# Kernel tuning notes

Measured on AMD Instinct MI355X. Metric: run time of the kernel, lower is better.

The kernel has to match this reference:

```python
import jax, jax.numpy as jnp
import numpy as np

HEADS = 8
HEAD_DIM = 64
SCALE = HEAD_DIM ** -0.5


def setup_inputs() -> dict:
    key = jax.random.key(0)
    k1, k2, k3 = jax.random.split(key, 3)
    b, p, n, dim = 8, 16, 256, 384
    inner = HEADS * HEAD_DIM  # 512
    x = jax.random.normal(k1, (b, p, n, dim), dtype=jnp.float32)
    w_qkv = jax.random.normal(k2, (dim, 3 * inner), dtype=jnp.float32) * (dim ** -0.5)
    w_out = jax.random.normal(k3, (inner, dim), dtype=jnp.float32) * (inner ** -0.5)
    b_out = jnp.zeros((dim,), dtype=jnp.float32)
    return {"x": x, "w_qkv": w_qkv, "w_out": w_out, "b_out": b_out}


def reference(x, w_qkv, w_out, b_out):
    b, p, n, dim = x.shape
    inner = HEADS * HEAD_DIM
    qkv = jnp.einsum('bpnd,de->bpne', x, w_qkv)  # [b,p,n,3*inner]
    q, k, v = jnp.split(qkv, 3, axis=-1)
    # [b,p,n,inner] -> [b,p,h,n,hd]
    def to_heads(t):
        return t.reshape(b, p, n, HEADS, HEAD_DIM).transpose(0, 1, 3, 2, 4)
    q, k, v = to_heads(q), to_heads(k), to_heads(v)
    dots = jnp.einsum('bphqd,bphkd->bphqk', q, k) * SCALE
    attn = jax.nn.softmax(dots, axis=-1)
    out = jnp.einsum('bphqk,bphkd->bphqd', attn, v)
    out = out.transpose(0, 1, 3, 2, 4).reshape(b, p, n, inner)
    return jnp.einsum('bpni,id->bpnd', out, w_out) + b_out
```

## Files before the change

### kernel.cpp

```cpp
#include <hip/hip_runtime.h>
#include <stdint.h>

#define DEVFN __device__ __forceinline__

typedef __attribute__((ext_vector_type(8))) __bf16 bf16x8;
typedef __attribute__((ext_vector_type(8))) short short8;
typedef __attribute__((ext_vector_type(4))) float f32x4;

DEVFN unsigned short f2bf(float f) {
  union { float f; unsigned u; } v; v.f = f;
  return (unsigned short)((v.u + 0x7FFFu + ((v.u >> 16) & 1u)) >> 16);
}

DEVFN void gload_lds16(const void* g, void* l) {
  __builtin_amdgcn_global_load_lds(
      (const __attribute__((address_space(1))) void*)(uintptr_t)g,
      (__attribute__((address_space(3))) void*)(uint32_t)(uintptr_t)l,
      16, 0, 0);
}


__global__ void k_cast_x(const float* __restrict__ x, short* __restrict__ xb, int n8) {
  int i = blockIdx.x * blockDim.x + threadIdx.x;
  if (i >= n8) return;
  const f32x4* xf = (const f32x4*)x;
  f32x4 a = xf[2 * i], b = xf[2 * i + 1];
  short8 s;
  s[0] = (short)f2bf(a[0]); s[1] = (short)f2bf(a[1]);
  s[2] = (short)f2bf(a[2]); s[3] = (short)f2bf(a[3]);
  s[4] = (short)f2bf(b[0]); s[5] = (short)f2bf(b[1]);
  s[6] = (short)f2bf(b[2]); s[7] = (short)f2bf(b[3]);
  ((short8*)xb)[i] = s;
}

__global__ void k_transpose_bf(const float* __restrict__ w, short* __restrict__ wt, int R, int C) {
  int i = blockIdx.x * blockDim.x + threadIdx.x;
  if (i >= R * C) return;
  int c = i / R, r = i - c * R;
  wt[i] = (short)f2bf(w[(size_t)r * C + c]);
}


template <int BF16_OUT>
__global__ __launch_bounds__(256, 3)
void k_gemm(const short* __restrict__ A, const short* __restrict__ Bt,
            unsigned short* __restrict__ Cb, float* __restrict__ Cf,
            const float* __restrict__ bias, int M, int N, int K) {
  __shared__ short As[3][128 * 32];
  __shared__ short Bs[3][128 * 32];
  const int tid = threadIdx.x;
  const int l = tid & 63, w = tid >> 6;
  const int ntile = N >> 7;
  const int nwg = gridDim.x, cpx = nwg >> 3;
  const int bid = (blockIdx.x & 7) * cpx + (blockIdx.x >> 3);
  const int mt = bid / ntile, nt = bid % ntile;
  const int m0 = mt << 7, n0 = nt << 7;
  const int wm = (w >> 1) << 6, wn = (w & 1) << 6;

  f32x4 acc[4][4];
#pragma unroll
  for (int i = 0; i < 4; i++)
#pragma unroll
    for (int j = 0; j < 4; j++) acc[i][j] = (f32x4){0.f, 0.f, 0.f, 0.f};

  const int nsteps = K >> 5;

  auto stage = [&](int buf, int t) {
#pragma unroll
    for (int c = 0; c < 2; ++c) {
      int ch = tid + c * 256;
      int row = ch >> 2, slot = ch & 3;
      gload_lds16(A + (size_t)(m0 + row) * K + t * 32 + slot * 8, &As[buf][ch * 8]);
      gload_lds16(Bt + (size_t)(n0 + row) * K + t * 32 + slot * 8, &Bs[buf][ch * 8]);
    }
  };
  auto compute = [&](int buf) {
    bf16x8 af[4], bfr[4];
#pragma unroll
    for (int i = 0; i < 4; i++) {
      af[i]  = *(const bf16x8*)&As[buf][(wm + i * 16 + (l & 15)) * 32 + (l >> 4) * 8];
      bfr[i] = *(const bf16x8*)&Bs[buf][(wn + i * 16 + (l & 15)) * 32 + (l >> 4) * 8];
    }
#pragma unroll
    for (int i = 0; i < 4; i++)
#pragma unroll
      for (int j = 0; j < 4; j++)
        acc[i][j] = __builtin_amdgcn_mfma_f32_16x16x32_bf16(af[i], bfr[j], acc[i][j], 0, 0, 0);
  };

  stage(0, 0);
  stage(1, 1);
#pragma unroll 1
  for (int t = 0; t < nsteps; ++t) {
    if (t + 1 < nsteps) {
      asm volatile("s_waitcnt vmcnt(4)" ::: "memory");
    } else {
      asm volatile("s_waitcnt vmcnt(0)" ::: "memory");
    }
    __builtin_amdgcn_sched_barrier(0);
    __builtin_amdgcn_s_barrier();
    __builtin_amdgcn_sched_barrier(0);
    if (t + 2 < nsteps) stage((t + 2) % 3, t + 2);
    compute(t % 3);
  }

#pragma unroll
  for (int i = 0; i < 4; i++) {
    int mrow = m0 + wm + i * 16 + ((l >> 4) << 2);
#pragma unroll
    for (int j = 0; j < 4; j++) {
      int ncol = n0 + wn + j * 16 + (l & 15);
#pragma unroll
      for (int r = 0; r < 4; r++) {
        if (BF16_OUT) {
          Cb[(size_t)(mrow + r) * N + ncol] = f2bf(acc[i][j][r]);
        } else {
          Cf[(size_t)(mrow + r) * N + ncol] = acc[i][j][r] + bias[ncol];
        }
      }
    }
  }
}


__global__ void k_attn(const short* __restrict__ qkv, unsigned short* __restrict__ O) {
  __shared__ short Kl[256 * 64];
  __shared__ short Vt[64 * 256];
  __shared__ short Pc[8][16 * 40];

  const int tid = threadIdx.x, l = tid & 63, w = tid >> 6;
  const int bh = blockIdx.x;
  const int bp = bh >> 3, h = bh & 7;
  const size_t tokbase = (size_t)bp * 256 * 1536;
  const int qoff = h * 64, koff = 512 + h * 64, voff = 1024 + h * 64;

#pragma unroll
  for (int c = 0; c < 4; ++c) {
    int ch = tid + c * 512;
    int row = ch >> 3, s = ch & 7;
    int sg = s ^ (row & 7);
    gload_lds16(qkv + tokbase + (size_t)row * 1536 + koff + sg * 8, &Kl[ch * 8]);
  }
#pragma unroll
  for (int c = 0; c < 4; ++c) {
    int ch = tid + c * 512;
    int row = ch >> 3, d0 = (ch & 7) * 8;
    short8 v = *(const short8*)(qkv + tokbase + (size_t)row * 1536 + voff + d0);
#pragma unroll
    for (int j = 0; j < 8; ++j) {
      int d = d0 + j;
      Vt[d * 256 + (((((row >> 3) ^ (d & 15))) << 3) | (row & 7))] = v[j];
    }
  }
  __syncthreads();

  const float CEXP = 0.125f * 1.44269504f;

#pragma unroll 1
  for (int it = 0; it < 2; ++it) {
    const int q0 = w * 32 + it * 16;
    bf16x8 qa[2];
#pragma unroll
    for (int dc = 0; dc < 2; ++dc)
      qa[dc] = *(const bf16x8*)(qkv + tokbase + (size_t)(q0 + (l & 15)) * 1536 + qoff +
                                dc * 32 + (l >> 4) * 8);
    f32x4 s[16];
#pragma unroll
    for (int kt = 0; kt < 16; kt++) s[kt] = (f32x4){0.f, 0.f, 0.f, 0.f};
#pragma unroll
    for (int dc = 0; dc < 2; ++dc) {
#pragma unroll
      for (int kt = 0; kt < 16; ++kt) {
        int kcol = kt * 16 + (l & 15);
        int sl = (dc * 4 + (l >> 4)) ^ (kcol & 7);
        bf16x8 kb = *(const bf16x8*)&Kl[kcol * 64 + sl * 8];
        s[kt] = __builtin_amdgcn_mfma_f32_16x16x32_bf16(qa[dc], kb, s[kt], 0, 0, 0);
      }
    }
    float rs[4];
#pragma unroll
    for (int r = 0; r < 4; ++r) {
      float m = s[0][r];
#pragma unroll
      for (int kt = 1; kt < 16; kt++) m = fmaxf(m, s[kt][r]);
      for (int off = 1; off < 16; off <<= 1) m = fmaxf(m, __shfl_xor(m, off, 64));
      float sum = 0.f;
#pragma unroll
      for (int kt = 0; kt < 16; kt++) {
        float p = exp2f((s[kt][r] - m) * CEXP);
        s[kt][r] = p;
        sum += p;
      }
      for (int off = 1; off < 16; off <<= 1) sum += __shfl_xor(sum, off, 64);
      rs[r] = 1.0f / sum;
    }
    f32x4 o[4];
#pragma unroll
    for (int dt = 0; dt < 4; dt++) o[dt] = (f32x4){0.f, 0.f, 0.f, 0.f};
    short* pc = &Pc[w][0];
#pragma unroll
    for (int kc = 0; kc < 8; ++kc) {
#pragma unroll
      for (int t2 = 0; t2 < 2; ++t2) {
        int kt = kc * 2 + t2;
#pragma unroll
        for (int r = 0; r < 4; ++r)
          pc[((l >> 4) * 4 + r) * 40 + t2 * 16 + (l & 15)] = (short)f2bf(s[kt][r]);
      }
      asm volatile("" ::: "memory");
      bf16x8 pa = *(const bf16x8*)&pc[(l & 15) * 40 + (l >> 4) * 8];
#pragma unroll
      for (int dt = 0; dt < 4; ++dt) {
        int d = dt * 16 + (l & 15);
        int sl = (kc * 4 + (l >> 4)) ^ (d & 15);
        bf16x8 vb = *(const bf16x8*)&Vt[d * 256 + sl * 8];
        o[dt] = __builtin_amdgcn_mfma_f32_16x16x32_bf16(pa, vb, o[dt], 0, 0, 0);
      }
      asm volatile("" ::: "memory");
    }
#pragma unroll
    for (int dt = 0; dt < 4; dt++) {
#pragma unroll
      for (int r = 0; r < 4; r++) {
        int qrow = q0 + ((l >> 4) << 2) + r;
        int d = dt * 16 + (l & 15);
        O[(size_t)(bp * 256 + qrow) * 512 + h * 64 + d] = f2bf(o[dt][r] * rs[r]);
      }
    }
  }
}


extern "C" void kernel_launch(void* const* d_in, const int* in_sizes, int n_in,
                              void* d_out, int out_size, void* d_ws, size_t ws_size,
                              hipStream_t stream) {
  const float* x    = (const float*)d_in[0];
  const float* wqkv = (const float*)d_in[1];
  const float* wout = (const float*)d_in[2];
  const float* bout = (const float*)d_in[3];
  float* out = (float*)d_out;
  char* ws = (char*)d_ws;

  short* Wot = (short*)(ws);
  short* Xb  = (short*)(ws + 393216);
  short* Wqt = (short*)(ws + 25559040);
  unsigned short* O = (unsigned short*)(ws + 393216);
  short* QKV = (short*)(ws + 33947648);

  k_cast_x<<<6144, 256, 0, stream>>>(x, Xb, 1572864);
  k_transpose_bf<<<2304, 256, 0, stream>>>(wqkv, Wqt, 384, 1536);
  k_transpose_bf<<<768, 256, 0, stream>>>(wout, Wot, 512, 384);
  k_gemm<1><<<3072, 256, 0, stream>>>(Xb, Wqt, (unsigned short*)QKV, nullptr, nullptr,
                                      32768, 1536, 384);
  k_attn<<<1024, 512, 0, stream>>>(QKV, O);
  k_gemm<0><<<768, 256, 0, stream>>>((const short*)O, Wot, nullptr, out, bout,
                                     32768, 384, 512);
  (void)in_sizes; (void)n_in; (void)out_size; (void)ws_size;
}
```

Measured before the change: 150.5 us.

## Load GEMM B operand directly into double-buffered registers, bypassing LDS

The weight (B) tile is no longer staged through shared memory. Each wave now loads its B fragments from global memory straight into registers, double-buffered across two register sets, while A keeps its three-stage LDS pipeline. The loop is unrolled by two and the vmcnt waits are adjusted for the extra in-flight loads. This halves LDS use and LDS read traffic per step, but waves sharing the same N columns now fetch B redundantly from cache and register pressure rises.

```diff
diff --git a/kernel.cpp b/kernel.cpp
--- a/kernel.cpp
+++ b/kernel.cpp
@@ -41,13 +41,45 @@
 }
 
 
+#define LOADB(DST, T)                                                              \
+  do {                                                                             \
+    _Pragma("unroll") for (int j_ = 0; j_ < 4; ++j_)                               \
+        DST[j_] = *(const bf16x8*)(Bt + (size_t)(n0 + wn + j_ * 16 + (l & 15)) * K \
+                                   + (T) * 32 + (l >> 4) * 8);                     \
+  } while (0)
+
+#define COMPUTE(BUF, BR)                                                           \
+  do {                                                                             \
+    bf16x8 af_[4];                                                                 \
+    _Pragma("unroll") for (int i_ = 0; i_ < 4; i_++)                               \
+        af_[i_] = *(const bf16x8*)&As[BUF][(wm + i_ * 16 + (l & 15)) * 32          \
+                                           + (l >> 4) * 8];                        \
+    _Pragma("unroll") for (int i_ = 0; i_ < 4; i_++)                               \
+        _Pragma("unroll") for (int j_ = 0; j_ < 4; j_++)                           \
+            acc[i_][j_] = __builtin_amdgcn_mfma_f32_16x16x32_bf16(                 \
+                af_[i_], BR[j_], acc[i_][j_], 0, 0, 0);                            \
+  } while (0)
+
+#define ITERSTEP(T, BCUR, BNXT)                                                    \
+  do {                                                                             \
+    const int t_ = (T);                                                            \
+    if (t_ + 1 < nsteps) LOADB(BNXT, t_ + 1);                                      \
+    if (t_ == 0)                asm volatile("s_waitcnt vmcnt(4)" ::: "memory");   \
+    else if (t_ + 1 < nsteps)   asm volatile("s_waitcnt vmcnt(6)" ::: "memory");   \
+    else                        asm volatile("s_waitcnt vmcnt(0)" ::: "memory");   \
+    __builtin_amdgcn_sched_barrier(0);                                             \
+    __builtin_amdgcn_s_barrier();                                                  \
+    __builtin_amdgcn_sched_barrier(0);                                             \
+    if (t_ + 2 < nsteps) stageA((t_ + 2) % 3, t_ + 2);                             \
+    COMPUTE(t_ % 3, BCUR);                                                         \
+  } while (0)
+
 template <int BF16_OUT>
 __global__ __launch_bounds__(256, 3)
 void k_gemm(const short* __restrict__ A, const short* __restrict__ Bt,
             unsigned short* __restrict__ Cb, float* __restrict__ Cf,
             const float* __restrict__ bias, int M, int N, int K) {
   __shared__ short As[3][128 * 32];
-  __shared__ short Bs[3][128 * 32];
   const int tid = threadIdx.x;
   const int l = tid & 63, w = tid >> 6;
   const int ntile = N >> 7;
@@ -65,43 +97,25 @@
 
   const int nsteps = K >> 5;
 
-  auto stage = [&](int buf, int t) {
+  auto stageA = [&](int buf, int t) {
 #pragma unroll
     for (int c = 0; c < 2; ++c) {
       int ch = tid + c * 256;
       int row = ch >> 2, slot = ch & 3;
       gload_lds16(A + (size_t)(m0 + row) * K + t * 32 + slot * 8, &As[buf][ch * 8]);
-      gload_lds16(Bt + (size_t)(n0 + row) * K + t * 32 + slot * 8, &Bs[buf][ch * 8]);
     }
   };
-  auto compute = [&](int buf) {
-    bf16x8 af[4], bfr[4];
-#pragma unroll
-    for (int i = 0; i < 4; i++) {
-      af[i]  = *(const bf16x8*)&As[buf][(wm + i * 16 + (l & 15)) * 32 + (l >> 4) * 8];
-      bfr[i] = *(const bf16x8*)&Bs[buf][(wn + i * 16 + (l & 15)) * 32 + (l >> 4) * 8];
-    }
-#pragma unroll
-    for (int i = 0; i < 4; i++)
-#pragma unroll
-      for (int j = 0; j < 4; j++)
-        acc[i][j] = __builtin_amdgcn_mfma_f32_16x16x32_bf16(af[i], bfr[j], acc[i][j], 0, 0, 0);
-  };
-
-  stage(0, 0);
-  stage(1, 1);
+
+  bf16x8 Bx[4], By[4];
+
+  stageA(0, 0);
+  stageA(1, 1);
+  LOADB(Bx, 0);
+
 #pragma unroll 1
-  for (int t = 0; t < nsteps; ++t) {
-    if (t + 1 < nsteps) {
-      asm volatile("s_waitcnt vmcnt(4)" ::: "memory");
-    } else {
-      asm volatile("s_waitcnt vmcnt(0)" ::: "memory");
-    }
-    __builtin_amdgcn_sched_barrier(0);
-    __builtin_amdgcn_s_barrier();
-    __builtin_amdgcn_sched_barrier(0);
-    if (t + 2 < nsteps) stage((t + 2) % 3, t + 2);
-    compute(t % 3);
+  for (int tp = 0; tp < nsteps; tp += 2) {
+    ITERSTEP(tp, Bx, By);
+    ITERSTEP(tp + 1, By, Bx);
   }
 
 #pragma unroll
```

After: 193.2 us. 1.28x slower.
